# Kernel optimization log

Hardware: AMD Instinct MI355X
Metric: run time of the kernel (lower is better)

## Reference

```python
import jax, jax.numpy as jnp
import numpy as np

# Model dims (match init_kwargs): dim=768, num_heads=12, num_kv_heads=2 -> G=6, head_dim=64
DIM, HKV, G, D = 768, 2, 6, 64


def setup_inputs() -> dict:
    key = jax.random.key(0)
    ks = jax.random.split(key, 9)
    w = 0.02  # init scale for weights
    return {
        "x": jax.random.normal(ks[0], (8, 1024, DIM), dtype=jnp.float32),
        "depth_k": jax.random.normal(ks[1], (8, 1024, HKV, D), dtype=jnp.float32),
        "depth_v": jax.random.normal(ks[2], (8, 1024, HKV, D), dtype=jnp.float32),
        "Wq": jax.random.normal(ks[3], (DIM, DIM), dtype=jnp.float32) * w,
        "bq": jnp.zeros((DIM,), dtype=jnp.float32),
        "Wkv": jax.random.normal(ks[4], (2 * HKV * D, DIM), dtype=jnp.float32) * w,
        "bkv": jnp.zeros((2 * HKV * D,), dtype=jnp.float32),
        "Wproj": jax.random.normal(ks[5], (DIM, DIM), dtype=jnp.float32) * w,
        "bproj": jnp.zeros((DIM,), dtype=jnp.float32),
    }


def reference(x, depth_k, depth_v, Wq, bq, Wkv, bkv, Wproj, bproj):
    B, N, C = x.shape
    scale = D ** -0.5
    # Q projection, GQA groups unfolded into the sequence dim: [B, N*G, Hkv, D]
    q = (x @ Wq.T + bq).reshape(B, N * G, HKV, D)
    # KV projection: [B, N, 2, Hkv, D]
    kv = (x @ Wkv.T + bkv).reshape(B, N, 2, HKV, D)
    k, v = kv[:, :, 0], kv[:, :, 1]
    # Concatenate depth (previous-layer) KV cache along the sequence dim
    k_full = jnp.concatenate([depth_k, k], axis=1)  # [B, N_cache+N, Hkv, D]
    v_full = jnp.concatenate([depth_v, v], axis=1)
    # Full (non-causal) attention per kv head over the unfolded query sequence
    scores = jnp.einsum('bqhd,bkhd->bhqk', q, k_full) * scale  # [B, Hkv, N*G, Kv]
    attn = jax.nn.softmax(scores, axis=-1)
    o = jnp.einsum('bhqk,bkhd->bqhd', attn, v_full)  # [B, N*G, Hkv, D]
    out = o.reshape(B, N, C) @ Wproj.T + bproj  # fold G*Hkv*D back to C=dim
    return out, k, v
```

## Files before the change

### kernel.cpp

```cpp
#include <hip/hip_runtime.h>

using sh8 = __attribute__((ext_vector_type(8))) short;
using sh4 = __attribute__((ext_vector_type(4))) short;
using fx4 = __attribute__((ext_vector_type(4))) float;

#define MFMA(a,b,c)   __builtin_amdgcn_mfma_f32_16x16x32_bf16((a),(b),(c),0,0,0)

__device__ __forceinline__ short f2bf(float f) {
    union { float f; unsigned u; } v; v.f = f;
    return (short)((v.u + 0x7fffu + ((v.u >> 16) & 1u)) >> 16);
}

__device__ __forceinline__ unsigned bfpair(float lo, float hi) {
    unsigned ul = __float_as_uint(lo) + 0x8000u;
    unsigned uh = __float_as_uint(hi) + 0x8000u;
    return __builtin_amdgcn_perm(uh, ul, 0x07060302);
}

__device__ __forceinline__ sh8 pack8(float4 a, float4 b) {
    union { unsigned u[4]; sh8 s; } r;
    r.u[0] = bfpair(a.x, a.y);
    r.u[1] = bfpair(a.z, a.w);
    r.u[2] = bfpair(b.x, b.y);
    r.u[3] = bfpair(b.z, b.w);
    return r.s;
}

#define QSCALE 0.18033688011112042f


__global__ __launch_bounds__(256) void prep_k(const float* __restrict__ x,
                                              const float* __restrict__ Wq,
                                              const float* __restrict__ bq,
                                              const float* __restrict__ Wkv,
                                              const float* __restrict__ bkv,
                                              const float* __restrict__ dk,
                                              const float* __restrict__ dv,
                                              float* __restrict__ ok,
                                              float* __restrict__ ov,
                                              short* __restrict__ q_ws,
                                              short* __restrict__ k_ws,
                                              short* __restrict__ vT_ws)
{
    __shared__ alignas(16) short Al[128 * 40];
    __shared__ alignas(16) short Bl[128 * 40];
    const int blk = blockIdx.x;
    const int t   = threadIdx.x;

    if (blk < 512) {
        const bool isq = (blk < 384);
        const int  i   = isq ? blk : blk - 384;
        const int  nbx = isq ? 6 : 2;
        const int  bm  = (i / nbx) * 128, bn = (i % nbx) * 128;
        const float* Wmat = isq ? Wq : Wkv;

        const int wave = t >> 6, lane = t & 63;
        const int wm   = wave >> 1, wn = wave & 1;
        const int lhi  = lane >> 4, llo = lane & 15;

        const int srow = t >> 1, scol = (t & 1) * 16;
        const float* ap = x    + (size_t)(bm + srow) * 768 + scol;
        const float* bp = Wmat + (size_t)(bn + srow) * 768 + scol;

        fx4 zero = {0.f, 0.f, 0.f, 0.f};
        fx4 acc[4][4];
        #pragma unroll
        for (int a = 0; a < 4; ++a)
            #pragma unroll
            for (int b2 = 0; b2 < 4; ++b2) acc[a][b2] = zero;

        float4 pa0 = *(const float4*)(ap);     float4 pa1 = *(const float4*)(ap + 4);
        float4 pa2 = *(const float4*)(ap + 8); float4 pa3 = *(const float4*)(ap + 12);
        float4 pb0 = *(const float4*)(bp);     float4 pb1 = *(const float4*)(bp + 4);
        float4 pb2 = *(const float4*)(bp + 8); float4 pb3 = *(const float4*)(bp + 12);

        for (int k0 = 0; k0 < 768; k0 += 32) {
            __syncthreads();
            *(sh8*)&Al[srow*40 + scol]     = pack8(pa0, pa1);
            *(sh8*)&Al[srow*40 + scol + 8] = pack8(pa2, pa3);
            *(sh8*)&Bl[srow*40 + scol]     = pack8(pb0, pb1);
            *(sh8*)&Bl[srow*40 + scol + 8] = pack8(pb2, pb3);
            __syncthreads();
            if (k0 + 32 < 768) {
                pa0 = *(const float4*)(ap + k0+32);  pa1 = *(const float4*)(ap + k0+36);
                pa2 = *(const float4*)(ap + k0+40);  pa3 = *(const float4*)(ap + k0+44);
                pb0 = *(const float4*)(bp + k0+32);  pb1 = *(const float4*)(bp + k0+36);
                pb2 = *(const float4*)(bp + k0+40);  pb3 = *(const float4*)(bp + k0+44);
            }
            sh8 af[4], bf[4];
            #pragma unroll
            for (int mt = 0; mt < 4; ++mt)
                af[mt] = *(const sh8*)&Al[(wm*64 + mt*16 + llo)*40 + lhi*8];
            #pragma unroll
            for (int nt = 0; nt < 4; ++nt)
                bf[nt] = *(const sh8*)&Bl[(wn*64 + nt*16 + llo)*40 + lhi*8];
            #pragma unroll
            for (int mt = 0; mt < 4; ++mt)
                #pragma unroll
                for (int nt = 0; nt < 4; ++nt)
                    acc[mt][nt] = MFMA(af[mt], bf[nt], acc[mt][nt]);
        }

        if (isq) {
            #pragma unroll
            for (int nt = 0; nt < 4; ++nt) {
                const int c = bn + wn*64 + nt*16 + llo;
                const float bias = bq[c];
                const int g = c >> 7, h = (c >> 6) & 1, d = c & 63;
                #pragma unroll
                for (int mt = 0; mt < 4; ++mt) {
                    const int m0 = bm + wm*64 + mt*16 + lhi*4;
                    #pragma unroll
                    for (int r = 0; r < 4; ++r) {
                        const int m = m0 + r;
                        const int b = m >> 10, n = m & 1023;
                        const float val = (acc[mt][nt][r] + bias) * QSCALE;
                        q_ws[((size_t)(b*2 + h)*6144 + n*6 + g)*64 + d] = f2bf(val);
                    }
                }
            }
        } else {
            #pragma unroll
            for (int nt = 0; nt < 4; ++nt) {
                const int c = bn + wn*64 + nt*16 + llo;
                const float bias = bkv[c];
                const int s = c >> 7, h = (c >> 6) & 1, d = c & 63;
                #pragma unroll
                for (int mt = 0; mt < 4; ++mt) {
                    const int m0 = bm + wm*64 + mt*16 + lhi*4;
                    const int b = m0 >> 10, n0 = m0 & 1023;
                    float vals[4];
                    #pragma unroll
                    for (int r = 0; r < 4; ++r) vals[r] = acc[mt][nt][r] + bias;
                    const int key = 1024 + n0;
                    if (s == 0) {
                        #pragma unroll
                        for (int r = 0; r < 4; ++r)
                            ok[((size_t)(b*1024 + n0 + r)*2 + h)*64 + d] = vals[r];
                        const int kb_ = key >> 6, nt_ = (key >> 4) & 3;
                        const int half = d >> 5, lhiK = (d >> 3) & 3, j = d & 7;
                        const size_t base = (size_t)(b*2 + h)*131072
                            + (size_t)(((((kb_*4 + nt_)*2 + half)*64) + lhiK*16 + (key & 15))*8 + j);
                        #pragma unroll
                        for (int r = 0; r < 4; ++r)
                            k_ws[base + r*8] = f2bf(vals[r]);
                    } else {
                        #pragma unroll
                        for (int r = 0; r < 4; ++r)
                            ov[((size_t)(b*1024 + n0 + r)*2 + h)*64 + d] = vals[r];
                        const int kb_ = key >> 6, g_ = (key >> 5) & 1, k5 = key & 31;
                        const int half5 = k5 >> 4, lhi5 = (k5 >> 2) & 3;
                        const int dt_ = d >> 4, llov = d & 15;
                        short4 pk = make_short4(f2bf(vals[0]), f2bf(vals[1]),
                                                f2bf(vals[2]), f2bf(vals[3]));
                        const size_t base = (size_t)(b*2 + h)*131072
                            + (size_t)(((((kb_*2 + g_)*4 + dt_)*64) + lhi5*16 + llov)*8 + half5*4);
                        *(short4*)&vT_ws[base] = pk;
                    }
                }
            }
        }
    } else if (blk < 1536) {
        const size_t idx4 = ((size_t)(blk - 512) * 256 + t) * 4;
        const int b  = (int)(idx4 >> 17);
        const int rm = (int)(idx4 & 131071);
        const int tt = rm >> 7, h = (rm >> 6) & 1, d = rm & 63;
        float4 v = *(const float4*)(dk + idx4);
        short4 pk = make_short4(f2bf(v.x), f2bf(v.y), f2bf(v.z), f2bf(v.w));
        const int kb_ = tt >> 6, nt_ = (tt >> 4) & 3, lloK = tt & 15;
        const int half = d >> 5, lhiK = (d >> 3) & 3, j = d & 7;
        const size_t addr = (size_t)(b*2 + h)*131072
            + (size_t)(((((kb_*4 + nt_)*2 + half)*64) + lhiK*16 + lloK)*8 + j);
        *(short4*)&k_ws[addr] = pk;
    } else {
        const int unit = (blk - 1536)*4 + (t >> 6);
        const int lane = t & 63, lhi = lane >> 4, llo = lane & 15;
        const int dt_ = unit & 3, g_ = (unit >> 2) & 1;
        const int kb_ = (unit >> 3) & 15, bh = unit >> 7;
        const int b = bh >> 1, h = bh & 1;
        const float* s0 = dv
            + ((size_t)((b*1024 + kb_*64 + g_*32 + lhi*4)*2 + h))*64 + dt_*16 + llo;
        union { short s[8]; sh8 v8; } o;
        #pragma unroll
        for (int jj = 0; jj < 4; ++jj) o.s[jj]     = f2bf(s0[(size_t)jj * 128]);
        #pragma unroll
        for (int jj = 0; jj < 4; ++jj) o.s[4 + jj] = f2bf(s0[(size_t)(16 + jj) * 128]);
        *(sh8*)&vT_ws[((size_t)bh*256 + (kb_*2 + g_)*4 + dt_)*512 + lane*8] = o.v8;
    }
}

__global__ __launch_bounds__(256) void attn_k(const short* __restrict__ q_ws,
                                              const short* __restrict__ k_ws,
                                              const short* __restrict__ vT_ws,
                                              short* __restrict__ o_ws)
{
    const int t    = threadIdx.x;
    const int wave = t >> 6, lane = t & 63;
    const int lhi  = lane >> 4, llo = lane & 15;
    const int bh   = blockIdx.y;
    const int b    = bh >> 1, h = bh & 1;
    const int qt   = blockIdx.x;

    const short* qb = q_ws + ((size_t)bh*6144 + qt*192 + wave*48) * 64;
    sh8 qf[3][2];
    #pragma unroll
    for (int s = 0; s < 3; ++s) {
        qf[s][0] = *(const sh8*)(qb + (s*16 + llo)*64 + lhi*8);
        qf[s][1] = *(const sh8*)(qb + (s*16 + llo)*64 + lhi*8 + 32);
    }

    const short* kp = k_ws  + (size_t)bh*131072 + lane*8;
    const short* vp = vT_ws + (size_t)bh*131072 + lane*8;

    fx4 zero = {0.f, 0.f, 0.f, 0.f};
    fx4 oacc[3][4];
    fx4 lacc[3];
    #pragma unroll
    for (int s = 0; s < 3; ++s) {
        lacc[s] = zero;
        #pragma unroll
        for (int dt = 0; dt < 4; ++dt) oacc[s][dt] = zero;
    }

    union { unsigned u[4]; sh8 s8; } onesu;
    onesu.u[0] = onesu.u[1] = onesu.u[2] = onesu.u[3] = 0x3F803F80u;
    const sh8 ones = onesu.s8;

    auto loadg = [&](sh8& K0, sh8& K1, sh8& K2, sh8& K3,
                     sh8& V0, sh8& V1, sh8& V2, sh8& V3, int it) {
        const short* kq = kp + (size_t)it * 2048;
        const short* vq = vp + (size_t)it * 2048;
        K0 = *(const sh8*)(kq);        K1 = *(const sh8*)(kq + 512);
        K2 = *(const sh8*)(kq + 1024); K3 = *(const sh8*)(kq + 1536);
        V0 = *(const sh8*)(vq);        V1 = *(const sh8*)(vq + 512);
        V2 = *(const sh8*)(vq + 1024); V3 = *(const sh8*)(vq + 1536);
    };

    auto compg = [&](sh8 K0, sh8 K1, sh8 K2, sh8 K3,
                     sh8 V0, sh8 V1, sh8 V2, sh8 V3) {
        #pragma unroll
        for (int s = 0; s < 3; ++s) {
            fx4 stA = MFMA(K0, qf[s][0], zero); stA = MFMA(K1, qf[s][1], stA);
            fx4 stB = MFMA(K2, qf[s][0], zero); stB = MFMA(K3, qf[s][1], stB);
            float pa0 = __builtin_amdgcn_exp2f(stA[0]);
            float pa1 = __builtin_amdgcn_exp2f(stA[1]);
            float pa2 = __builtin_amdgcn_exp2f(stA[2]);
            float pa3 = __builtin_amdgcn_exp2f(stA[3]);
            float pb0 = __builtin_amdgcn_exp2f(stB[0]);
            float pb1 = __builtin_amdgcn_exp2f(stB[1]);
            float pb2 = __builtin_amdgcn_exp2f(stB[2]);
            float pb3 = __builtin_amdgcn_exp2f(stB[3]);
            union { unsigned u[4]; sh8 s8; } pu;
            pu.u[0] = bfpair(pa0, pa1);
            pu.u[1] = bfpair(pa2, pa3);
            pu.u[2] = bfpair(pb0, pb1);
            pu.u[3] = bfpair(pb2, pb3);
            lacc[s]    = MFMA(pu.s8, ones, lacc[s]);
            oacc[s][0] = MFMA(pu.s8, V0, oacc[s][0]);
            oacc[s][1] = MFMA(pu.s8, V1, oacc[s][1]);
            oacc[s][2] = MFMA(pu.s8, V2, oacc[s][2]);
            oacc[s][3] = MFMA(pu.s8, V3, oacc[s][3]);
        }
    };

    sh8 xk0, xk1, xk2, xk3, xv0, xv1, xv2, xv3;
    sh8 yk0, yk1, yk2, yk3, yv0, yv1, yv2, yv3;

    loadg(xk0, xk1, xk2, xk3, xv0, xv1, xv2, xv3, 0);
    for (int it = 0; it < 64; it += 2) {
        loadg(yk0, yk1, yk2, yk3, yv0, yv1, yv2, yv3, it + 1);
        compg(xk0, xk1, xk2, xk3, xv0, xv1, xv2, xv3);
        loadg(xk0, xk1, xk2, xk3, xv0, xv1, xv2, xv3, (it + 2 < 64) ? it + 2 : 63);
        compg(yk0, yk1, yk2, yk3, yv0, yv1, yv2, yv3);
    }

    #pragma unroll
    for (int s = 0; s < 3; ++s) {
        #pragma unroll
        for (int r = 0; r < 4; ++r) {
            const float iq = 1.0f / lacc[s][r];
            const int qi = qt*192 + wave*48 + s*16 + lhi*4 + r;
            const int n = qi / 6, g = qi % 6;
            short* orow = o_ws + ((size_t)(b*1024 + n))*768 + g*128 + h*64;
            #pragma unroll
            for (int dt = 0; dt < 4; ++dt)
                orow[dt*16 + llo] = f2bf(oacc[s][dt][r] * iq);
        }
    }
}

__global__ __launch_bounds__(256) void projgemm_k(const short* __restrict__ o_ws,
                                                  const float* __restrict__ Wp,
                                                  const float* __restrict__ bpj,
                                                  float* __restrict__ out)
{
    __shared__ alignas(16) short Al[128 * 40];
    __shared__ alignas(16) short Bl[128 * 40];
    const int t    = threadIdx.x;
    const int wave = t >> 6, lane = t & 63;
    const int wm   = wave >> 1, wn = wave & 1;
    const int lhi  = lane >> 4, llo = lane & 15;
    const int bm   = blockIdx.y * 128, bn = blockIdx.x * 128;

    const int srow = t >> 1, scol = (t & 1) * 16;
    const short* ap = o_ws + (size_t)(bm + srow) * 768 + scol;
    const float* bp = Wp   + (size_t)(bn + srow) * 768 + scol;

    fx4 zero = {0.f, 0.f, 0.f, 0.f};
    fx4 acc[4][4];
    #pragma unroll
    for (int i = 0; i < 4; ++i)
        #pragma unroll
        for (int j = 0; j < 4; ++j) acc[i][j] = zero;

    sh8 qa0 = *(const sh8*)(ap), qa1 = *(const sh8*)(ap + 8);
    float4 pb0 = *(const float4*)(bp);     float4 pb1 = *(const float4*)(bp + 4);
    float4 pb2 = *(const float4*)(bp + 8); float4 pb3 = *(const float4*)(bp + 12);

    for (int k0 = 0; k0 < 768; k0 += 32) {
        __syncthreads();
        *(sh8*)&Al[srow*40 + scol]     = qa0;
        *(sh8*)&Al[srow*40 + scol + 8] = qa1;
        *(sh8*)&Bl[srow*40 + scol]     = pack8(pb0, pb1);
        *(sh8*)&Bl[srow*40 + scol + 8] = pack8(pb2, pb3);
        __syncthreads();
        if (k0 + 32 < 768) {
            qa0 = *(const sh8*)(ap + k0+32);  qa1 = *(const sh8*)(ap + k0+40);
            pb0 = *(const float4*)(bp + k0+32);  pb1 = *(const float4*)(bp + k0+36);
            pb2 = *(const float4*)(bp + k0+40);  pb3 = *(const float4*)(bp + k0+44);
        }
        sh8 af[4], bf[4];
        #pragma unroll
        for (int mt = 0; mt < 4; ++mt)
            af[mt] = *(const sh8*)&Al[(wm*64 + mt*16 + llo)*40 + lhi*8];
        #pragma unroll
        for (int nt = 0; nt < 4; ++nt)
            bf[nt] = *(const sh8*)&Bl[(wn*64 + nt*16 + llo)*40 + lhi*8];
        #pragma unroll
        for (int mt = 0; mt < 4; ++mt)
            #pragma unroll
            for (int nt = 0; nt < 4; ++nt)
                acc[mt][nt] = MFMA(af[mt], bf[nt], acc[mt][nt]);
    }

    #pragma unroll
    for (int nt = 0; nt < 4; ++nt) {
        const int c = bn + wn*64 + nt*16 + llo;
        const float bias = bpj[c];
        #pragma unroll
        for (int mt = 0; mt < 4; ++mt) {
            const int m0 = bm + wm*64 + mt*16 + lhi*4;
            #pragma unroll
            for (int r = 0; r < 4; ++r)
                out[(size_t)(m0 + r)*768 + c] = acc[mt][nt][r] + bias;
        }
    }
}

extern "C" void kernel_launch(void* const* d_in, const int* in_sizes, int n_in,
                              void* d_out, int out_size, void* d_ws, size_t ws_size,
                              hipStream_t stream)
{
    const float* x   = (const float*)d_in[0];
    const float* dk  = (const float*)d_in[1];
    const float* dv  = (const float*)d_in[2];
    const float* Wq  = (const float*)d_in[3];
    const float* bq  = (const float*)d_in[4];
    const float* Wkv = (const float*)d_in[5];
    const float* bkv = (const float*)d_in[6];
    const float* Wp  = (const float*)d_in[7];
    const float* bpj = (const float*)d_in[8];

    float* out = (float*)d_out;
    float* ok  = out + 6291456;
    float* ov  = out + 7340032;

    char* ws = (char*)d_ws;
    short* q_ws  = (short*)(ws);
    short* k_ws  = (short*)(ws + 12582912);
    short* vT_ws = (short*)(ws + 16777216);
    short* o_ws  = (short*)(ws + 20971520);

    prep_k     <<<dim3(2048),   256, 0, stream>>>(x, Wq, bq, Wkv, bkv, dk, dv,
                                                  ok, ov, q_ws, k_ws, vT_ws);
    attn_k     <<<dim3(32, 16), 256, 0, stream>>>(q_ws, k_ws, vT_ws, o_ws);
    projgemm_k <<<dim3(6, 64),  256, 0, stream>>>(o_ws, Wp, bpj, out);
}
```

Before: 213.3 us.

## Stage shared K/V tiles in LDS via async global-to-LDS loads

```diff
diff --git a/kernel.cpp b/kernel.cpp
--- a/kernel.cpp
+++ b/kernel.cpp
@@ -27,6 +27,10 @@
 }
 
 #define QSCALE 0.18033688011112042f
+
+#define GLOAD_LDS16(gsrc, ldst) __builtin_amdgcn_global_load_lds( \
+    (const __attribute__((address_space(1))) void*)(gsrc),        \
+    (__attribute__((address_space(3))) void*)(ldst), 16, 0, 0)
 
 
 __global__ __launch_bounds__(256) void prep_k(const float* __restrict__ x,
@@ -194,6 +198,7 @@
                                               const short* __restrict__ vT_ws,
                                               short* __restrict__ o_ws)
 {
+    __shared__ alignas(16) short L[4][8][512];
     const int t    = threadIdx.x;
     const int wave = t >> 6, lane = t & 63;
     const int lhi  = lane >> 4, llo = lane & 15;
@@ -209,8 +214,8 @@
         qf[s][1] = *(const sh8*)(qb + (s*16 + llo)*64 + lhi*8 + 32);
     }
 
-    const short* kp = k_ws  + (size_t)bh*131072 + lane*8;
-    const short* vp = vT_ws + (size_t)bh*131072 + lane*8;
+    const short* kbase = k_ws  + (size_t)bh*131072;
+    const short* vbase = vT_ws + (size_t)bh*131072;
 
     fx4 zero = {0.f, 0.f, 0.f, 0.f};
     fx4 oacc[3][4];
@@ -226,18 +231,39 @@
     onesu.u[0] = onesu.u[1] = onesu.u[2] = onesu.u[3] = 0x3F803F80u;
     const sh8 ones = onesu.s8;
 
-    auto loadg = [&](sh8& K0, sh8& K1, sh8& K2, sh8& K3,
-                     sh8& V0, sh8& V1, sh8& V2, sh8& V3, int it) {
-        const short* kq = kp + (size_t)it * 2048;
-        const short* vq = vp + (size_t)it * 2048;
-        K0 = *(const sh8*)(kq);        K1 = *(const sh8*)(kq + 512);
-        K2 = *(const sh8*)(kq + 1024); K3 = *(const sh8*)(kq + 1536);
-        V0 = *(const sh8*)(vq);        V1 = *(const sh8*)(vq + 512);
-        V2 = *(const sh8*)(vq + 1024); V3 = *(const sh8*)(vq + 1536);
+    auto stage = [&](int g) {
+        const short* ks = kbase + ((size_t)g*4 + wave)*512 + lane*8;
+        const short* vs = vbase + ((size_t)g*4 + wave)*512 + lane*8;
+        GLOAD_LDS16(ks, &L[g & 3][wave][0]);
+        GLOAD_LDS16(vs, &L[g & 3][4 + wave][0]);
     };
 
-    auto compg = [&](sh8 K0, sh8 K1, sh8 K2, sh8 K3,
-                     sh8 V0, sh8 V1, sh8 V2, sh8 V3) {
+    stage(0);
+    stage(1);
+
+    for (int g = 0; g < 64; ++g) {
+        if (g < 62) {
+            stage(g + 2);
+            asm volatile("s_waitcnt vmcnt(4)" ::: "memory");
+        } else if (g == 62) {
+            asm volatile("s_waitcnt vmcnt(2)" ::: "memory");
+        } else {
+            asm volatile("s_waitcnt vmcnt(0)" ::: "memory");
+        }
+        __builtin_amdgcn_s_barrier();
+        __builtin_amdgcn_sched_barrier(0);
+
+        const short* Lb = (const short*)&L[g & 3][0][0];
+        const int lo = lane * 8;
+        sh8 K0 = *(const sh8*)(Lb + lo);
+        sh8 K1 = *(const sh8*)(Lb + 512  + lo);
+        sh8 K2 = *(const sh8*)(Lb + 1024 + lo);
+        sh8 K3 = *(const sh8*)(Lb + 1536 + lo);
+        sh8 V0 = *(const sh8*)(Lb + 2048 + lo);
+        sh8 V1 = *(const sh8*)(Lb + 2560 + lo);
+        sh8 V2 = *(const sh8*)(Lb + 3072 + lo);
+        sh8 V3 = *(const sh8*)(Lb + 3584 + lo);
+
         #pragma unroll
         for (int s = 0; s < 3; ++s) {
             fx4 stA = MFMA(K0, qf[s][0], zero); stA = MFMA(K1, qf[s][1], stA);
@@ -261,17 +287,6 @@
             oacc[s][2] = MFMA(pu.s8, V2, oacc[s][2]);
             oacc[s][3] = MFMA(pu.s8, V3, oacc[s][3]);
         }
-    };
-
-    sh8 xk0, xk1, xk2, xk3, xv0, xv1, xv2, xv3;
-    sh8 yk0, yk1, yk2, yk3, yv0, yv1, yv2, yv3;
-
-    loadg(xk0, xk1, xk2, xk3, xv0, xv1, xv2, xv3, 0);
-    for (int it = 0; it < 64; it += 2) {
-        loadg(yk0, yk1, yk2, yk3, yv0, yv1, yv2, yv3, it + 1);
-        compg(xk0, xk1, xk2, xk3, xv0, xv1, xv2, xv3);
-        loadg(xk0, xk1, xk2, xk3, xv0, xv1, xv2, xv3, (it + 2 < 64) ? it + 2 : 63);
-        compg(yk0, yk1, yk2, yk3, yv0, yv1, yv2, yv3);
     }
 
     #pragma unroll
```

Result: no change. 214.1 us (+0.4%).
